# Optimization experiments

Measured on AMD Instinct MI355X. Metric: run time of the kernel, lower is better.

## Reference

```python
import jax, jax.numpy as jnp
import numpy as np

B, S, D = 8, 2048, 1024

def setup_inputs() -> dict:
    key = jax.random.key(0)
    kq, kk, kv = jax.random.split(key, 3)
    qm = jax.random.normal(kq, (B, S, D), dtype=jnp.float32)
    km = jax.random.normal(kk, (B, S, D), dtype=jnp.float32)
    vm = jax.random.normal(kv, (B, S, D), dtype=jnp.float32)
    return {"qm": qm, "km": km, "vm": vm}

def reference(qm, km, vm):
    # qkm = qm @ km^T / sqrt(d_k)   -> [B, S, S]
    scale = 1.0 / jnp.sqrt(jnp.asarray(qm.shape[-1], dtype=qm.dtype))
    qkm = jnp.einsum('bqd,bkd->bqk', qm, km) * scale
    # NOTE: faithful to source: softmax is applied AFTER the second matmul,
    # i.e. softmax((QK^T/sqrt(d)) @ V, axis=-1). masking=False (module default).
    out = jnp.einsum('bqk,bkd->bqd', qkm, vm)  # [B, S, D]
    return jax.nn.softmax(out, axis=-1)
```

## Files before the change

kernel.cpp:

```cpp
#include <hip/hip_runtime.h>
#include <hip/hip_bf16.h>
#include <stdint.h>

#define BATCH 8
#define SEQ   2048
#define DIM   1024

typedef unsigned short u16;
typedef __attribute__((ext_vector_type(8))) short short8;
typedef __attribute__((ext_vector_type(4))) float f32x4;
typedef __attribute__((ext_vector_type(4))) unsigned short us4;

__device__ __forceinline__ u16 f2bf(float x){
  union { float f; uint32_t u; } c; c.f = x;
  uint32_t u = c.u;
  uint32_t r = u + 0x7fffu + ((u >> 16) & 1u);
  return (u16)(r >> 16);
}
__device__ __forceinline__ float bf2f(u16 s){
  union { uint32_t u; float f; } c; c.u = ((uint32_t)s) << 16;
  return c.f;
}

__device__ __forceinline__ void gload16(const void* g, void* l){
  __builtin_amdgcn_global_load_lds(
      (const __attribute__((address_space(1))) void*)g,
      (__attribute__((address_space(3))) void*)l, 16, 0, 0);
}

__global__ __launch_bounds__(256) void k_split(const float* __restrict__ src,
                                               u16* __restrict__ dst, int nchunk){
  for (int i = blockIdx.x*blockDim.x + threadIdx.x; i < nchunk; i += gridDim.x*blockDim.x){
    int r = i >> 8;
    int c = (i & 255) << 2;
    f32x4 v = *(const f32x4*)(src + (size_t)r*DIM + c);
    us4 h, l;
    #pragma unroll
    for (int j = 0; j < 4; j++){
      u16 hh = f2bf(v[j]);
      h[j] = hh;
      l[j] = f2bf(v[j] - bf2f(hh));
    }
    u16* d = dst + (size_t)r*(2*DIM) + c;
    *(us4*)d         = h;
    *(us4*)(d + DIM) = l;
  }
}

__global__ __launch_bounds__(256) void k_convert_kv(const float* __restrict__ K,
                                                    const float* __restrict__ V,
                                                    u16* __restrict__ Kt,
                                                    u16* __restrict__ Vt){
  __shared__ float tile[64][65];
  int z = blockIdx.z;
  const float* Src = (z < 8 ? K : V);
  u16* Dst = (z < 8 ? Kt : Vt);
  int zb = z & 7;
  const float* Vb = Src + (size_t)zb * SEQ * DIM;
  u16* Vtb = Dst + (size_t)zb * DIM * (2*SEQ);
  int s0 = blockIdx.x * 64, d0 = blockIdx.y * 64;
  int t = threadIdx.x;
  int rs = t >> 4;
  int cd = (t & 15) * 4;
  #pragma unroll
  for (int i = 0; i < 4; i++){
    int s = rs + i*16;
    f32x4 v = *(const f32x4*)(Vb + (size_t)(s0 + s)*DIM + d0 + cd);
    tile[s][cd+0] = v[0]; tile[s][cd+1] = v[1];
    tile[s][cd+2] = v[2]; tile[s][cd+3] = v[3];
  }
  __syncthreads();
  int dl = t >> 4;
  int sl = (t & 15) * 4;
  #pragma unroll
  for (int i = 0; i < 4; i++){
    int d = dl + i*16;
    us4 h, l;
    #pragma unroll
    for (int j = 0; j < 4; j++){
      float x = tile[sl+j][d];
      u16 hh = f2bf(x);
      h[j] = hh;
      l[j] = f2bf(x - bf2f(hh));
    }
    size_t off = (size_t)(d0 + d) * (2*SEQ) + s0 + sl;
    *(us4*)(Vtb + off)       = h;
    *(us4*)(Vtb + off + SEQ) = l;
  }
}

template<int N_, int KB, int SPLITOUT, int BX, int RX, int RY>
__global__ __launch_bounds__(256,2) void k_gemm(const u16* __restrict__ A,
                                                const u16* __restrict__ B,
                                                void* __restrict__ Cout,
                                                size_t aStride, size_t bStride, size_t cStride){
  constexpr int LA = 2*KB;
  __shared__ __align__(16) u16 lds[2][4][128*32];

  int orig = blockIdx.x;
  int xcd = orig & 7;
  int idx = orig >> 3;
  constexpr int RN = RX * RY;
  int z  = idx / RN;
  int r  = idx % RN;
  int bx = (xcd % (BX/RX)) * RX + (r % RX);
  int by = (xcd / (BX/RX)) * RY + (r / RX);

  const u16* Ab = A + (size_t)z * aStride;
  const u16* Bb = B + (size_t)z * bStride;

  int t = threadIdx.x, lane = t & 63, w = t >> 6;
  int wm = (w & 1) * 64, wn = (w >> 1) * 64;
  int fr = lane & 15;

  int srow    = lane >> 2;
  int srcSlot = ((lane & 3) ^ ((lane >> 3) & 3)) * 8;

  const u16* aBase = Ab + ((size_t)bx*128) * LA + srcSlot;
  const u16* bBase = Bb + ((size_t)by*128) * LA + srcSlot;

  int rdSlot = (((lane >> 4) ^ ((fr >> 1) & 3))) * 8;

  f32x4 acc[4][4] = {};

  #define STAGE(buf, k0)                                                      \
    { _Pragma("unroll")                                                       \
      for (int o = 0; o < 2; o++){                                            \
        int c = w*2 + o;                                                      \
        size_t rOff = (size_t)(c*16 + srow) * LA + (k0);                      \
        const u16* ga = aBase + rOff;                                         \
        const u16* gb = bBase + rOff;                                         \
        int le = c * 512;                                                     \
        gload16(ga,      &lds[buf][0][le]);                                   \
        gload16(ga + KB, &lds[buf][1][le]);                                   \
        gload16(gb,      &lds[buf][2][le]);                                   \
        gload16(gb + KB, &lds[buf][3][le]);                                   \
      } }

  #define COMPUTE(buf)                                                        \
    { short8 fah[4], fal[4], fbh[4], fbl[4];                                  \
      _Pragma("unroll")                                                       \
      for (int mi = 0; mi < 4; mi++){                                         \
        fah[mi] = *(const short8*)&lds[buf][0][(wm + mi*16 + fr)*32 + rdSlot];\
        fal[mi] = *(const short8*)&lds[buf][1][(wm + mi*16 + fr)*32 + rdSlot];\
        fbh[mi] = *(const short8*)&lds[buf][2][(wn + mi*16 + fr)*32 + rdSlot];\
        fbl[mi] = *(const short8*)&lds[buf][3][(wn + mi*16 + fr)*32 + rdSlot];\
      }                                                                       \
      _Pragma("unroll")                                                       \
      for (int mi = 0; mi < 4; mi++){                                         \
        _Pragma("unroll")                                                     \
        for (int ni = 0; ni < 4; ni++){                                       \
          acc[mi][ni] = __builtin_amdgcn_mfma_f32_16x16x32_bf16(fah[mi], fbh[ni], acc[mi][ni], 0,0,0); \
          acc[mi][ni] = __builtin_amdgcn_mfma_f32_16x16x32_bf16(fah[mi], fbl[ni], acc[mi][ni], 0,0,0); \
          acc[mi][ni] = __builtin_amdgcn_mfma_f32_16x16x32_bf16(fal[mi], fbh[ni], acc[mi][ni], 0,0,0); \
        }                                                                     \
      } }

  STAGE(0, 0)
  int cur = 0;
  for (int k0 = 0; k0 + 32 < KB; k0 += 32, cur ^= 1){
    STAGE(cur^1, k0 + 32)
    asm volatile("s_waitcnt vmcnt(8)" ::: "memory");
    __builtin_amdgcn_sched_barrier(0);
    __builtin_amdgcn_s_barrier();
    __builtin_amdgcn_sched_barrier(0);
    COMPUTE(cur)
    __builtin_amdgcn_sched_barrier(0);
    __builtin_amdgcn_s_barrier();
  }
  asm volatile("s_waitcnt vmcnt(0)" ::: "memory");
  __builtin_amdgcn_sched_barrier(0);
  __builtin_amdgcn_s_barrier();
  __builtin_amdgcn_sched_barrier(0);
  COMPUTE(cur)

  #undef STAGE
  #undef COMPUTE

  int cr = (lane >> 4) * 4, cc = lane & 15;
  if (SPLITOUT){
    u16* Cb = (u16*)Cout + (size_t)z * cStride;
    const float scale = 0.03125f;
    #pragma unroll
    for (int mi = 0; mi < 4; mi++){
      int gr = bx*128 + wm + mi*16 + cr;
      #pragma unroll
      for (int ni = 0; ni < 4; ni++){
        int gc = by*128 + wn + ni*16 + cc;
        #pragma unroll
        for (int rr = 0; rr < 4; rr++){
          float x = acc[mi][ni][rr] * scale;
          u16 h = f2bf(x);
          u16 l = f2bf(x - bf2f(h));
          size_t off = (size_t)(gr + rr) * (2*N_) + gc;
          Cb[off]      = h;
          Cb[off + N_] = l;
        }
      }
    }
  } else {
    float* Cb = (float*)Cout + (size_t)z * cStride;
    #pragma unroll
    for (int mi = 0; mi < 4; mi++){
      int gr = bx*128 + wm + mi*16 + cr;
      #pragma unroll
      for (int ni = 0; ni < 4; ni++){
        int gc = by*128 + wn + ni*16 + cc;
        #pragma unroll
        for (int rr = 0; rr < 4; rr++){
          Cb[(size_t)(gr + rr) * N_ + gc] = acc[mi][ni][rr];
        }
      }
    }
  }
}

__global__ __launch_bounds__(256) void k_softmax(float* __restrict__ O){
  float* p = O + (size_t)blockIdx.x * DIM;
  int t = threadIdx.x;
  int lane = t & 63, wave = t >> 6;
  f32x4 v = *(f32x4*)(p + t*4);
  float m = fmaxf(fmaxf(v[0], v[1]), fmaxf(v[2], v[3]));
  #pragma unroll
  for (int o = 32; o > 0; o >>= 1) m = fmaxf(m, __shfl_xor(m, o));
  __shared__ float rmax[4], rsum[4];
  if (lane == 0) rmax[wave] = m;
  __syncthreads();
  m = fmaxf(fmaxf(rmax[0], rmax[1]), fmaxf(rmax[2], rmax[3]));
  float e0 = expf(v[0]-m), e1 = expf(v[1]-m), e2 = expf(v[2]-m), e3 = expf(v[3]-m);
  float s = e0 + e1 + e2 + e3;
  #pragma unroll
  for (int o = 32; o > 0; o >>= 1) s += __shfl_xor(s, o);
  if (lane == 0) rsum[wave] = s;
  __syncthreads();
  s = rsum[0] + rsum[1] + rsum[2] + rsum[3];
  float inv = 1.0f / s;
  f32x4 rv = { e0*inv, e1*inv, e2*inv, e3*inv };
  *(f32x4*)(p + t*4) = rv;
}

extern "C" void kernel_launch(void* const* d_in, const int* in_sizes, int n_in,
                              void* d_out, int out_size, void* d_ws, size_t ws_size,
                              hipStream_t stream){
  const float* Q = (const float*)d_in[0];
  const float* K = (const float*)d_in[1];
  const float* V = (const float*)d_in[2];
  float* Out = (float*)d_out;
  u16* w = (u16*)d_ws;

  const size_t QsB = (size_t)SEQ * (2*DIM);
  const size_t KtB = (size_t)DIM * (2*SEQ);
  const size_t VtB = KtB;
  const size_t WsB = (size_t)DIM * (2*DIM);

  dim3 blk(256);
  dim3 cgrid(SEQ/64, DIM/64, 16);

  const size_t need1 = 8 * (QsB + KtB + VtB + WsB) * sizeof(u16);
  const size_t need2 = 8 * (KtB + VtB + WsB) * sizeof(u16);

  if (ws_size >= need1){
    u16* Qs = w;
    u16* Kt = Qs + 8*QsB;
    u16* Vt = Kt + 8*KtB;
    u16* Ws = Vt + 8*VtB;
    k_split<<<dim3(2048), blk, 0, stream>>>(Q, Qs, 8*SEQ*(DIM/4));
    k_convert_kv<<<cgrid, blk, 0, stream>>>(K, V, Kt, Vt);
    k_gemm<DIM, SEQ, 1, 8, 2, 4><<<dim3(512), blk, 0, stream>>>(Vt, Kt, Ws, VtB, KtB, WsB);
    k_gemm<DIM, DIM, 0, 16, 4, 4><<<dim3(1024), blk, 0, stream>>>(Qs, Ws, Out, QsB, WsB, (size_t)SEQ*DIM);
  } else if (ws_size >= need2){
    u16* Kt = w;
    u16* Vt = Kt + 8*KtB;
    u16* Ws = Vt + 8*VtB;
    u16* Qs = w;
    k_convert_kv<<<cgrid, blk, 0, stream>>>(K, V, Kt, Vt);
    k_gemm<DIM, SEQ, 1, 8, 2, 4><<<dim3(512), blk, 0, stream>>>(Vt, Kt, Ws, VtB, KtB, WsB);
    k_split<<<dim3(2048), blk, 0, stream>>>(Q, Qs, 8*SEQ*(DIM/4));
    k_gemm<DIM, DIM, 0, 16, 4, 4><<<dim3(1024), blk, 0, stream>>>(Qs, Ws, Out, QsB, WsB, (size_t)SEQ*DIM);
  } else {
    u16* Qs = w;
    u16* Kt = Qs + QsB;
    u16* Vt = Kt + KtB;
    u16* Ws = Vt + VtB;
    dim3 cg1(SEQ/64, DIM/64, 2);
    for (int b = 0; b < BATCH; b++){
      const size_t inOff = (size_t)b * SEQ * DIM;
      k_split<<<dim3(1024), blk, 0, stream>>>(Q + inOff, Qs, SEQ*(DIM/4));
      k_convert_kv<<<dim3(SEQ/64, DIM/64, 1), blk, 0, stream>>>(K + inOff, K + inOff, Kt, Kt);
      k_convert_kv<<<dim3(SEQ/64, DIM/64, 1), blk, 0, stream>>>(V + inOff, V + inOff, Vt, Vt);
      k_gemm<DIM, SEQ, 1, 8, 2, 4><<<dim3(64), blk, 0, stream>>>(Vt, Kt, Ws, VtB, KtB, WsB);
      k_gemm<DIM, DIM, 0, 16, 4, 4><<<dim3(128), blk, 0, stream>>>(Qs, Ws, Out + inOff, QsB, WsB, (size_t)SEQ*DIM);
    }
  }
  k_softmax<<<dim3(BATCH*SEQ), blk, 0, stream>>>(Out);
}
```

Measured before the change: 309.4 us.

## Add 256x256-tile 8-wave GEMM with split-K for KᵀV and reduce kernel

Adds a new GEMM kernel using 512-thread blocks computing 256x256 output tiles with a finer-grained interleaving of LDS fragment loads and MFMA groups, barriers and wave priority raising. The KᵀV product is split into two K-halves written as fp32 partials, then a new reduce kernel sums them, applies the scale, and splits into bf16 hi/lo. The Q·W product also uses the new big-tile kernel. The aim is more operand reuse per tile and better MFMA occupancy, at the cost of an extra partial buffer round-trip, a new launch, and one block per CU with high register pressure.

```diff
diff --git a/kernel.cpp b/kernel.cpp
--- a/kernel.cpp
+++ b/kernel.cpp
@@ -89,11 +89,170 @@
   }
 }
 
+template<int KROW, int SPLITK, int TPZX, int TPZY>
+__global__ __launch_bounds__(512,1) void k_gemm8(const u16* __restrict__ A,
+                                                 const u16* __restrict__ B,
+                                                 float* __restrict__ C,
+                                                 size_t aStride, size_t bStride, size_t cStride){
+  constexpr int LA = 2*KROW;
+  constexpr int NT = 1024/32;
+  __shared__ __align__(16) u16 lds[2][4][256*32];
+
+  int xcd = blockIdx.x & 7;
+  int idx = blockIdx.x >> 3;
+  int nPerX = gridDim.x >> 3;
+  int gid = xcd * nPerX + idx;
+  constexpr int TPZ = TPZX*TPZY;
+  int z  = gid / TPZ;
+  int rm = gid % TPZ;
+  int bx = rm % TPZX;
+  int by = rm / TPZX;
+
+  int zb = SPLITK ? (z & 7) : z;
+  int kh = SPLITK ? (z >> 3) : 0;
+
+  const u16* Ab = A + (size_t)zb * aStride + (size_t)kh * 1024;
+  const u16* Bb = B + (size_t)zb * bStride + (size_t)kh * 1024;
+  float* Cb = C + (size_t)z * cStride;
+
+  int t0 = threadIdx.x, lane = t0 & 63, wv = t0 >> 6;
+  int wm = (wv >> 2) * 128, wn = (wv & 3) * 64;
+  int fr = lane & 15;
+  int rdSlot = ((lane >> 4) ^ ((fr >> 1) & 3)) * 8;
+  int srow = lane >> 2;
+  int srcSlot = ((lane & 3) ^ ((lane >> 3) & 3)) * 8;
+
+  const u16* aB = Ab + ((size_t)bx*256) * LA + srcSlot;
+  const u16* bB = Bb + ((size_t)by*256) * LA + srcSlot;
+  int ldsB0 = wv*512;
+
+  f32x4 acc[8][4] = {};
+  short8 fah[4], fal[4], fbh0[2], fbl0[2], fbh1[2], fbl1[2];
+
+  #define STAGE8(buf, t32)                                                    \
+    { _Pragma("unroll")                                                       \
+      for (int hf = 0; hf < 2; hf++){                                         \
+        size_t ro = (size_t)(wv*16 + hf*128 + srow) * LA + (size_t)(t32)*32;  \
+        const u16* ga = aB + ro;                                              \
+        const u16* gb = bB + ro;                                              \
+        int lo = ldsB0 + hf*4096;                                             \
+        gload16(ga,        &lds[buf][0][lo]);                                 \
+        gload16(ga + KROW, &lds[buf][1][lo]);                                 \
+        gload16(gb,        &lds[buf][2][lo]);                                 \
+        gload16(gb + KROW, &lds[buf][3][lo]);                                 \
+      } }
+
+  #define LOAD_A(buf, h)                                                      \
+    { _Pragma("unroll")                                                       \
+      for (int q = 0; q < 4; q++){                                            \
+        int ra = (wm + ((h)*4+q)*16 + fr)*32 + rdSlot;                        \
+        fah[q] = *(const short8*)&lds[buf][0][ra];                            \
+        fal[q] = *(const short8*)&lds[buf][1][ra];                            \
+      } }
+  #define LOAD_B0(buf)                                                        \
+    { _Pragma("unroll")                                                       \
+      for (int q = 0; q < 2; q++){                                            \
+        int rb = (wn + q*16 + fr)*32 + rdSlot;                                \
+        fbh0[q] = *(const short8*)&lds[buf][2][rb];                           \
+        fbl0[q] = *(const short8*)&lds[buf][3][rb];                           \
+      } }
+  #define LOAD_B1(buf)                                                        \
+    { _Pragma("unroll")                                                       \
+      for (int q = 0; q < 2; q++){                                            \
+        int rb = (wn + (2+q)*16 + fr)*32 + rdSlot;                            \
+        fbh1[q] = *(const short8*)&lds[buf][2][rb];                           \
+        fbl1[q] = *(const short8*)&lds[buf][3][rb];                           \
+      } }
+
+  #define MFMA_Q(h, bh, bl, nb)                                               \
+    { _Pragma("unroll")                                                       \
+      for (int q = 0; q < 4; q++){                                            \
+        _Pragma("unroll")                                                     \
+        for (int j = 0; j < 2; j++){                                          \
+          f32x4 a0 = acc[(h)*4+q][(nb)+j];                                    \
+          a0 = __builtin_amdgcn_mfma_f32_16x16x32_bf16(fah[q], bh[j], a0, 0,0,0); \
+          a0 = __builtin_amdgcn_mfma_f32_16x16x32_bf16(fah[q], bl[j], a0, 0,0,0); \
+          a0 = __builtin_amdgcn_mfma_f32_16x16x32_bf16(fal[q], bh[j], a0, 0,0,0); \
+          acc[(h)*4+q][(nb)+j] = a0;                                          \
+        } } }
+
+  #define BARR()  __builtin_amdgcn_s_barrier()
+  #define LGKM0() { asm volatile("s_waitcnt lgkmcnt(0)" ::: "memory"); __builtin_amdgcn_sched_barrier(0); }
+  #define VMC0()  { asm volatile("s_waitcnt vmcnt(0)" ::: "memory"); __builtin_amdgcn_sched_barrier(0); }
+
+  STAGE8(0, 0)
+  VMC0()
+  BARR();
+
+  for (int t = 0; t < NT; t++){
+    int buf = t & 1;
+    if (t+1 < NT) STAGE8(buf^1, t+1)
+    LOAD_A(buf, 0) LOAD_B0(buf)
+    BARR(); LGKM0()
+    __builtin_amdgcn_s_setprio(1); MFMA_Q(0, fbh0, fbl0, 0) __builtin_amdgcn_s_setprio(0);
+    BARR();
+    LOAD_B1(buf)
+    BARR(); LGKM0()
+    __builtin_amdgcn_s_setprio(1); MFMA_Q(0, fbh1, fbl1, 2) __builtin_amdgcn_s_setprio(0);
+    BARR();
+    LOAD_A(buf, 1)
+    BARR(); LGKM0()
+    __builtin_amdgcn_s_setprio(1); MFMA_Q(1, fbh1, fbl1, 2) __builtin_amdgcn_s_setprio(0);
+    BARR();
+    __builtin_amdgcn_s_setprio(1); MFMA_Q(1, fbh0, fbl0, 0) __builtin_amdgcn_s_setprio(0);
+    if (t+1 < NT) VMC0()
+    BARR();
+  }
+
+  #undef STAGE8
+  #undef LOAD_A
+  #undef LOAD_B0
+  #undef LOAD_B1
+  #undef MFMA_Q
+  #undef BARR
+  #undef LGKM0
+  #undef VMC0
+
+  int cr = (lane >> 4) * 4;
+  #pragma unroll
+  for (int mi = 0; mi < 8; mi++){
+    int gr = bx*256 + wm + mi*16 + cr;
+    #pragma unroll
+    for (int ni = 0; ni < 4; ni++){
+      int gc = by*256 + wn + ni*16 + fr;
+      #pragma unroll
+      for (int e = 0; e < 4; e++)
+        Cb[(size_t)(gr + e) * 1024 + gc] = acc[mi][ni][e];
+    }
+  }
+}
+
+__global__ __launch_bounds__(256) void k_reduce_split(const float* __restrict__ P,
+                                                      u16* __restrict__ Ws){
+  int i = blockIdx.x*256 + threadIdx.x;
+  int rg = i >> 8;
+  int c  = (i & 255) * 4;
+  f32x4 a = *(const f32x4*)(P + (size_t)rg*1024 + c);
+  f32x4 b = *(const f32x4*)(P + ((size_t)rg + 8192)*1024 + c);
+  us4 h, l;
+  #pragma unroll
+  for (int j = 0; j < 4; j++){
+    float x = (a[j] + b[j]) * 0.03125f;
+    u16 hh = f2bf(x);
+    h[j] = hh;
+    l[j] = f2bf(x - bf2f(hh));
+  }
+  int zb = rg >> 10, d = rg & 1023;
+  u16* Wb = Ws + (size_t)zb * ((size_t)DIM * 2*DIM);
+  *(us4*)(Wb + (size_t)d*2048 + c)        = h;
+  *(us4*)(Wb + (size_t)d*2048 + 1024 + c) = l;
+}
+
 template<int N_, int KB, int SPLITOUT, int BX, int RX, int RY>
-__global__ __launch_bounds__(256,2) void k_gemm(const u16* __restrict__ A,
-                                                const u16* __restrict__ B,
-                                                void* __restrict__ Cout,
-                                                size_t aStride, size_t bStride, size_t cStride){
+__global__ __launch_bounds__(256,2) void k_gemm2ph(const u16* __restrict__ A,
+                                                   const u16* __restrict__ B,
+                                                   void* __restrict__ Cout,
+                                                   size_t aStride, size_t bStride, size_t cStride){
   constexpr int LA = 2*KB;
   __shared__ __align__(16) u16 lds[2][4][128*32];
 
@@ -112,13 +271,11 @@
   int t = threadIdx.x, lane = t & 63, w = t >> 6;
   int wm = (w & 1) * 64, wn = (w >> 1) * 64;
   int fr = lane & 15;
-
   int srow    = lane >> 2;
   int srcSlot = ((lane & 3) ^ ((lane >> 3) & 3)) * 8;
 
   const u16* aBase = Ab + ((size_t)bx*128) * LA + srcSlot;
   const u16* bBase = Bb + ((size_t)by*128) * LA + srcSlot;
-
   int rdSlot = (((lane >> 4) ^ ((fr >> 1) & 3))) * 8;
 
   f32x4 acc[4][4] = {};
@@ -256,40 +413,45 @@
   dim3 blk(256);
   dim3 cgrid(SEQ/64, DIM/64, 16);
 
-  const size_t need1 = 8 * (QsB + KtB + VtB + WsB) * sizeof(u16);
-  const size_t need2 = 8 * (KtB + VtB + WsB) * sizeof(u16);
-
-  if (ws_size >= need1){
-    u16* Qs = w;
-    u16* Kt = Qs + 8*QsB;
+  const size_t base2 = 8 * (KtB + VtB + WsB) * sizeof(u16);
+  const size_t needA = base2 + (size_t)16*1024*1024*sizeof(float);
+  const size_t needB = base2;
+
+  if (ws_size >= needA){
+    u16* Kt = w;
     u16* Vt = Kt + 8*KtB;
     u16* Ws = Vt + 8*VtB;
+    float* Part = (float*)(Ws + 8*WsB);
+    u16* Qs = w;
+    k_convert_kv<<<cgrid, blk, 0, stream>>>(K, V, Kt, Vt);
+    k_gemm8<SEQ, 1, 4, 4><<<dim3(256), dim3(512), 0, stream>>>(
+        Vt, Kt, Part, VtB, KtB, (size_t)1024*1024);
+    k_reduce_split<<<dim3(8192), blk, 0, stream>>>(Part, Ws);
     k_split<<<dim3(2048), blk, 0, stream>>>(Q, Qs, 8*SEQ*(DIM/4));
-    k_convert_kv<<<cgrid, blk, 0, stream>>>(K, V, Kt, Vt);
-    k_gemm<DIM, SEQ, 1, 8, 2, 4><<<dim3(512), blk, 0, stream>>>(Vt, Kt, Ws, VtB, KtB, WsB);
-    k_gemm<DIM, DIM, 0, 16, 4, 4><<<dim3(1024), blk, 0, stream>>>(Qs, Ws, Out, QsB, WsB, (size_t)SEQ*DIM);
-  } else if (ws_size >= need2){
+    k_gemm8<DIM, 0, 8, 4><<<dim3(256), dim3(512), 0, stream>>>(
+        Qs, Ws, Out, QsB, WsB, (size_t)SEQ*DIM);
+  } else if (ws_size >= needB){
     u16* Kt = w;
     u16* Vt = Kt + 8*KtB;
     u16* Ws = Vt + 8*VtB;
     u16* Qs = w;
     k_convert_kv<<<cgrid, blk, 0, stream>>>(K, V, Kt, Vt);
-    k_gemm<DIM, SEQ, 1, 8, 2, 4><<<dim3(512), blk, 0, stream>>>(Vt, Kt, Ws, VtB, KtB, WsB);
+    k_gemm2ph<DIM, SEQ, 1, 8, 2, 4><<<dim3(512), blk, 0, stream>>>(Vt, Kt, Ws, VtB, KtB, WsB);
     k_split<<<dim3(2048), blk, 0, stream>>>(Q, Qs, 8*SEQ*(DIM/4));
-    k_gemm<DIM, DIM, 0, 16, 4, 4><<<dim3(1024), blk, 0, stream>>>(Qs, Ws, Out, QsB, WsB, (size_t)SEQ*DIM);
+    k_gemm8<DIM, 0, 8, 4><<<dim3(256), dim3(512), 0, stream>>>(
+        Qs, Ws, Out, QsB, WsB, (size_t)SEQ*DIM);
   } else {
     u16* Qs = w;
     u16* Kt = Qs + QsB;
     u16* Vt = Kt + KtB;
     u16* Ws = Vt + VtB;
-    dim3 cg1(SEQ/64, DIM/64, 2);
     for (int b = 0; b < BATCH; b++){
       const size_t inOff = (size_t)b * SEQ * DIM;
       k_split<<<dim3(1024), blk, 0, stream>>>(Q + inOff, Qs, SEQ*(DIM/4));
       k_convert_kv<<<dim3(SEQ/64, DIM/64, 1), blk, 0, stream>>>(K + inOff, K + inOff, Kt, Kt);
       k_convert_kv<<<dim3(SEQ/64, DIM/64, 1), blk, 0, stream>>>(V + inOff, V + inOff, Vt, Vt);
-      k_gemm<DIM, SEQ, 1, 8, 2, 4><<<dim3(64), blk, 0, stream>>>(Vt, Kt, Ws, VtB, KtB, WsB);
-      k_gemm<DIM, DIM, 0, 16, 4, 4><<<dim3(128), blk, 0, stream>>>(Qs, Ws, Out + inOff, QsB, WsB, (size_t)SEQ*DIM);
+      k_gemm2ph<DIM, SEQ, 1, 8, 2, 4><<<dim3(64), blk, 0, stream>>>(Vt, Kt, Ws, VtB, KtB, WsB);
+      k_gemm2ph<DIM, DIM, 0, 16, 4, 4><<<dim3(128), blk, 0, stream>>>(Qs, Ws, Out + inOff, QsB, WsB, (size_t)SEQ*DIM);
     }
   }
   k_softmax<<<dim3(BATCH*SEQ), blk, 0, stream>>>(Out);
```

Measured after the change: 285.4 us. 7.8% less time.

## Enlarge GEMM tiles to 128/256x256 with wave-level sub-blocking and drop Q-split-first path

Applied to the files above, without the earlier changes.

Replaces the 128x128-tile split-bf16 GEMM with a templated kernel that uses 128x256 or 256x256 block tiles, one block per CU, and 64x128 or 128x128 per-wave tiles. A and B fragments are loaded in sub-blocks to limit register pressure. The larger tiles raise arithmetic intensity and cut LDS and global traffic per MFMA. The cost is fewer blocks (256), which gives coarser load balance across CUs, plus higher register use and lower occupancy. The workspace path that split Q before computing K^T V is removed, so the smaller-workspace ordering is now always used.

```diff
diff --git a/kernel.cpp b/kernel.cpp
--- a/kernel.cpp
+++ b/kernel.cpp
@@ -26,6 +26,13 @@
   __builtin_amdgcn_global_load_lds(
       (const __attribute__((address_space(1))) void*)g,
       (__attribute__((address_space(3))) void*)l, 16, 0, 0);
+}
+
+__device__ __forceinline__ f32x4 mfma3(short8 ah, short8 al, short8 bh, short8 bl, f32x4 c){
+  c = __builtin_amdgcn_mfma_f32_16x16x32_bf16(ah, bh, c, 0,0,0);
+  c = __builtin_amdgcn_mfma_f32_16x16x32_bf16(ah, bl, c, 0,0,0);
+  c = __builtin_amdgcn_mfma_f32_16x16x32_bf16(al, bh, c, 0,0,0);
+  return c;
 }
 
 __global__ __launch_bounds__(256) void k_split(const float* __restrict__ src,
@@ -89,127 +96,158 @@
   }
 }
 
-template<int N_, int KB, int SPLITOUT, int BX, int RX, int RY>
-__global__ __launch_bounds__(256,2) void k_gemm(const u16* __restrict__ A,
-                                                const u16* __restrict__ B,
-                                                void* __restrict__ Cout,
-                                                size_t aStride, size_t bStride, size_t cStride){
-  constexpr int LA = 2*KB;
-  __shared__ __align__(16) u16 lds[2][4][128*32];
-
-  int orig = blockIdx.x;
-  int xcd = orig & 7;
-  int idx = orig >> 3;
-  constexpr int RN = RX * RY;
-  int z  = idx / RN;
-  int r  = idx % RN;
-  int bx = (xcd % (BX/RX)) * RX + (r % RX);
-  int by = (xcd / (BX/RX)) * RY + (r / RX);
+template<int BM, int KROW, int SPLITOUT, int NOUT, int TPZX, int TPZY>
+__global__ __launch_bounds__(256,1) void k_gemm4(const u16* __restrict__ A,
+                                                 const u16* __restrict__ B,
+                                                 void* __restrict__ Cout,
+                                                 size_t aStride, size_t bStride, size_t cStride){
+  constexpr int LA  = 2*KROW;
+  constexpr int NT  = KROW/32;
+  constexpr int AF  = BM/32;
+  constexpr int NAG = AF/4;
+  constexpr int ACH = BM/64;
+  constexpr int NLD = 2*ACH + 8;
+  constexpr int OAL = BM*32;
+  constexpr int OBH = 2*BM*32;
+  constexpr int OBL = 2*BM*32 + 8192;
+  constexpr int LDSPB = 2*BM*32 + 16384;
+
+  __shared__ __align__(16) u16 lds[2][LDSPB];
+
+  int xcd = blockIdx.x & 7;
+  int idx = blockIdx.x >> 3;
+  int nPerX = gridDim.x >> 3;
+  int gid = xcd * nPerX + idx;
+  constexpr int TPZ = TPZX*TPZY;
+  int z  = gid / TPZ;
+  int rm = gid % TPZ;
+  int bx = rm % TPZX;
+  int by = rm / TPZX;
 
   const u16* Ab = A + (size_t)z * aStride;
   const u16* Bb = B + (size_t)z * bStride;
 
-  int t = threadIdx.x, lane = t & 63, w = t >> 6;
-  int wm = (w & 1) * 64, wn = (w >> 1) * 64;
+  int t0 = threadIdx.x, lane = t0 & 63, wv = t0 >> 6;
+  int wm = (wv >> 1) * (BM/2);
+  int wn = (wv & 1) * 128;
   int fr = lane & 15;
-
-  int srow    = lane >> 2;
+  int rdSlot = ((lane >> 4) ^ ((fr >> 1) & 3)) * 8;
+  int srow4 = lane >> 2;
   int srcSlot = ((lane & 3) ^ ((lane >> 3) & 3)) * 8;
 
-  const u16* aBase = Ab + ((size_t)bx*128) * LA + srcSlot;
-  const u16* bBase = Bb + ((size_t)by*128) * LA + srcSlot;
-
-  int rdSlot = (((lane >> 4) ^ ((fr >> 1) & 3))) * 8;
-
-  f32x4 acc[4][4] = {};
-
-  #define STAGE(buf, k0)                                                      \
-    { _Pragma("unroll")                                                       \
-      for (int o = 0; o < 2; o++){                                            \
-        int c = w*2 + o;                                                      \
-        size_t rOff = (size_t)(c*16 + srow) * LA + (k0);                      \
-        const u16* ga = aBase + rOff;                                         \
-        const u16* gb = bBase + rOff;                                         \
-        int le = c * 512;                                                     \
-        gload16(ga,      &lds[buf][0][le]);                                   \
-        gload16(ga + KB, &lds[buf][1][le]);                                   \
-        gload16(gb,      &lds[buf][2][le]);                                   \
-        gload16(gb + KB, &lds[buf][3][le]);                                   \
-      } }
-
-  #define COMPUTE(buf)                                                        \
-    { short8 fah[4], fal[4], fbh[4], fbl[4];                                  \
+  const u16* aB = Ab + ((size_t)bx*BM)  * LA + srcSlot;
+  const u16* bB = Bb + ((size_t)by*256) * LA + srcSlot;
+
+  f32x4 acc[AF][8] = {};
+  short8 aH[4], aL[4], bH[4], bL[4];
+
+  #define STAGE(buf, t32)                                                     \
+    { size_t kof = (size_t)(t32)*32;                                          \
       _Pragma("unroll")                                                       \
-      for (int mi = 0; mi < 4; mi++){                                         \
-        fah[mi] = *(const short8*)&lds[buf][0][(wm + mi*16 + fr)*32 + rdSlot];\
-        fal[mi] = *(const short8*)&lds[buf][1][(wm + mi*16 + fr)*32 + rdSlot];\
-        fbh[mi] = *(const short8*)&lds[buf][2][(wn + mi*16 + fr)*32 + rdSlot];\
-        fbl[mi] = *(const short8*)&lds[buf][3][(wn + mi*16 + fr)*32 + rdSlot];\
+      for (int c = 0; c < ACH; c++){                                          \
+        size_t ro = (size_t)(c*64 + wv*16 + srow4)*LA + kof;                  \
+        gload16(aB + ro,        &lds[buf][      c*2048 + wv*512]);            \
+        gload16(aB + KROW + ro, &lds[buf][OAL + c*2048 + wv*512]);            \
       }                                                                       \
       _Pragma("unroll")                                                       \
-      for (int mi = 0; mi < 4; mi++){                                         \
+      for (int c = 0; c < 4; c++){                                            \
+        size_t ro = (size_t)(c*64 + wv*16 + srow4)*LA + kof;                  \
+        gload16(bB + ro,        &lds[buf][OBH + c*2048 + wv*512]);            \
+        gload16(bB + KROW + ro, &lds[buf][OBL + c*2048 + wv*512]);            \
+      } }
+
+  #define LOAD_A(buf, ag)                                                     \
+    { _Pragma("unroll")                                                       \
+      for (int q = 0; q < 4; q++){                                            \
+        int ra = (wm + (ag)*64 + q*16 + fr)*32 + rdSlot;                      \
+        aH[q] = *(const short8*)&lds[buf][ra];                                \
+        aL[q] = *(const short8*)&lds[buf][OAL + ra];                          \
+      } }
+  #define LOAD_B(buf, bh)                                                     \
+    { _Pragma("unroll")                                                       \
+      for (int q = 0; q < 4; q++){                                            \
+        int rb = (wn + (bh)*64 + q*16 + fr)*32 + rdSlot;                      \
+        bH[q] = *(const short8*)&lds[buf][OBH + rb];                          \
+        bL[q] = *(const short8*)&lds[buf][OBL + rb];                          \
+      } }
+  #define MFMA_BLK(ag, bh)                                                    \
+    { _Pragma("unroll")                                                       \
+      for (int q = 0; q < 4; q++){                                            \
         _Pragma("unroll")                                                     \
-        for (int ni = 0; ni < 4; ni++){                                       \
-          acc[mi][ni] = __builtin_amdgcn_mfma_f32_16x16x32_bf16(fah[mi], fbh[ni], acc[mi][ni], 0,0,0); \
-          acc[mi][ni] = __builtin_amdgcn_mfma_f32_16x16x32_bf16(fah[mi], fbl[ni], acc[mi][ni], 0,0,0); \
-          acc[mi][ni] = __builtin_amdgcn_mfma_f32_16x16x32_bf16(fal[mi], fbh[ni], acc[mi][ni], 0,0,0); \
-        }                                                                     \
-      } }
+        for (int j = 0; j < 4; j++){                                          \
+          acc[(ag)*4+q][(bh)*4+j] =                                           \
+            mfma3(aH[q], aL[q], bH[j], bL[j], acc[(ag)*4+q][(bh)*4+j]);       \
+        } } }
+
+  #define SB0() __builtin_amdgcn_sched_barrier(0)
 
   STAGE(0, 0)
-  int cur = 0;
-  for (int k0 = 0; k0 + 32 < KB; k0 += 32, cur ^= 1){
-    STAGE(cur^1, k0 + 32)
-    asm volatile("s_waitcnt vmcnt(8)" ::: "memory");
-    __builtin_amdgcn_sched_barrier(0);
+  asm volatile("s_waitcnt vmcnt(0)" ::: "memory");
+  __builtin_amdgcn_s_barrier();
+  SB0();
+
+  for (int t = 0; t < NT; t++){
+    int buf = t & 1;
+    if (t+1 < NT){
+      STAGE(buf^1, t+1)
+      asm volatile("s_waitcnt vmcnt(%0)" :: "i"(NLD) : "memory");
+    } else {
+      asm volatile("s_waitcnt vmcnt(0)" ::: "memory");
+    }
     __builtin_amdgcn_s_barrier();
-    __builtin_amdgcn_sched_barrier(0);
-    COMPUTE(cur)
-    __builtin_amdgcn_sched_barrier(0);
+    SB0();
+    #pragma unroll
+    for (int bh = 0; bh < 2; bh++){
+      LOAD_B(buf, bh)
+      #pragma unroll
+      for (int ag = 0; ag < NAG; ag++){
+        LOAD_A(buf, ag)
+        MFMA_BLK(ag, bh)
+      }
+    }
+    SB0();
     __builtin_amdgcn_s_barrier();
-  }
-  asm volatile("s_waitcnt vmcnt(0)" ::: "memory");
-  __builtin_amdgcn_sched_barrier(0);
-  __builtin_amdgcn_s_barrier();
-  __builtin_amdgcn_sched_barrier(0);
-  COMPUTE(cur)
+    SB0();
+  }
 
   #undef STAGE
-  #undef COMPUTE
-
-  int cr = (lane >> 4) * 4, cc = lane & 15;
+  #undef LOAD_A
+  #undef LOAD_B
+  #undef MFMA_BLK
+  #undef SB0
+
+  int cr = (lane >> 4) * 4;
   if (SPLITOUT){
     u16* Cb = (u16*)Cout + (size_t)z * cStride;
     const float scale = 0.03125f;
     #pragma unroll
-    for (int mi = 0; mi < 4; mi++){
-      int gr = bx*128 + wm + mi*16 + cr;
+    for (int mi = 0; mi < AF; mi++){
+      int gr = bx*BM + wm + mi*16 + cr;
       #pragma unroll
-      for (int ni = 0; ni < 4; ni++){
-        int gc = by*128 + wn + ni*16 + cc;
+      for (int ni = 0; ni < 8; ni++){
+        int gc = by*256 + wn + ni*16 + fr;
         #pragma unroll
-        for (int rr = 0; rr < 4; rr++){
-          float x = acc[mi][ni][rr] * scale;
+        for (int e = 0; e < 4; e++){
+          float x = acc[mi][ni][e] * scale;
           u16 h = f2bf(x);
           u16 l = f2bf(x - bf2f(h));
-          size_t off = (size_t)(gr + rr) * (2*N_) + gc;
-          Cb[off]      = h;
-          Cb[off + N_] = l;
+          size_t off = (size_t)(gr + e) * (2*NOUT) + gc;
+          Cb[off]        = h;
+          Cb[off + NOUT] = l;
         }
       }
     }
   } else {
     float* Cb = (float*)Cout + (size_t)z * cStride;
     #pragma unroll
-    for (int mi = 0; mi < 4; mi++){
-      int gr = bx*128 + wm + mi*16 + cr;
+    for (int mi = 0; mi < AF; mi++){
+      int gr = bx*BM + wm + mi*16 + cr;
       #pragma unroll
-      for (int ni = 0; ni < 4; ni++){
-        int gc = by*128 + wn + ni*16 + cc;
+      for (int ni = 0; ni < 8; ni++){
+        int gc = by*256 + wn + ni*16 + fr;
         #pragma unroll
-        for (int rr = 0; rr < 4; rr++){
-          Cb[(size_t)(gr + rr) * N_ + gc] = acc[mi][ni][rr];
-        }
+        for (int e = 0; e < 4; e++)
+          Cb[(size_t)(gr + e) * NOUT + gc] = acc[mi][ni][e];
       }
     }
   }
@@ -256,40 +294,33 @@
   dim3 blk(256);
   dim3 cgrid(SEQ/64, DIM/64, 16);
 
-  const size_t need1 = 8 * (QsB + KtB + VtB + WsB) * sizeof(u16);
-  const size_t need2 = 8 * (KtB + VtB + WsB) * sizeof(u16);
-
-  if (ws_size >= need1){
-    u16* Qs = w;
-    u16* Kt = Qs + 8*QsB;
-    u16* Vt = Kt + 8*KtB;
-    u16* Ws = Vt + 8*VtB;
-    k_split<<<dim3(2048), blk, 0, stream>>>(Q, Qs, 8*SEQ*(DIM/4));
-    k_convert_kv<<<cgrid, blk, 0, stream>>>(K, V, Kt, Vt);
-    k_gemm<DIM, SEQ, 1, 8, 2, 4><<<dim3(512), blk, 0, stream>>>(Vt, Kt, Ws, VtB, KtB, WsB);
-    k_gemm<DIM, DIM, 0, 16, 4, 4><<<dim3(1024), blk, 0, stream>>>(Qs, Ws, Out, QsB, WsB, (size_t)SEQ*DIM);
-  } else if (ws_size >= need2){
+  const size_t need = 8 * (KtB + VtB + WsB) * sizeof(u16);
+
+  if (ws_size >= need){
     u16* Kt = w;
     u16* Vt = Kt + 8*KtB;
     u16* Ws = Vt + 8*VtB;
     u16* Qs = w;
     k_convert_kv<<<cgrid, blk, 0, stream>>>(K, V, Kt, Vt);
-    k_gemm<DIM, SEQ, 1, 8, 2, 4><<<dim3(512), blk, 0, stream>>>(Vt, Kt, Ws, VtB, KtB, WsB);
+    k_gemm4<128, SEQ, 1, DIM, 8, 4><<<dim3(256), blk, 0, stream>>>(
+        Vt, Kt, Ws, VtB, KtB, WsB);
     k_split<<<dim3(2048), blk, 0, stream>>>(Q, Qs, 8*SEQ*(DIM/4));
-    k_gemm<DIM, DIM, 0, 16, 4, 4><<<dim3(1024), blk, 0, stream>>>(Qs, Ws, Out, QsB, WsB, (size_t)SEQ*DIM);
+    k_gemm4<256, DIM, 0, DIM, 8, 4><<<dim3(256), blk, 0, stream>>>(
+        Qs, Ws, Out, QsB, WsB, (size_t)SEQ*DIM);
   } else {
     u16* Qs = w;
     u16* Kt = Qs + QsB;
     u16* Vt = Kt + KtB;
     u16* Ws = Vt + VtB;
-    dim3 cg1(SEQ/64, DIM/64, 2);
     for (int b = 0; b < BATCH; b++){
       const size_t inOff = (size_t)b * SEQ * DIM;
       k_split<<<dim3(1024), blk, 0, stream>>>(Q + inOff, Qs, SEQ*(DIM/4));
       k_convert_kv<<<dim3(SEQ/64, DIM/64, 1), blk, 0, stream>>>(K + inOff, K + inOff, Kt, Kt);
       k_convert_kv<<<dim3(SEQ/64, DIM/64, 1), blk, 0, stream>>>(V + inOff, V + inOff, Vt, Vt);
-      k_gemm<DIM, SEQ, 1, 8, 2, 4><<<dim3(64), blk, 0, stream>>>(Vt, Kt, Ws, VtB, KtB, WsB);
-      k_gemm<DIM, DIM, 0, 16, 4, 4><<<dim3(128), blk, 0, stream>>>(Qs, Ws, Out + inOff, QsB, WsB, (size_t)SEQ*DIM);
+      k_gemm4<128, SEQ, 1, DIM, 8, 4><<<dim3(32), blk, 0, stream>>>(
+          Vt, Kt, Ws, VtB, KtB, WsB);
+      k_gemm4<256, DIM, 0, DIM, 8, 4><<<dim3(32), blk, 0, stream>>>(
+          Qs, Ws, Out + inOff, QsB, WsB, (size_t)SEQ*DIM);
     }
   }
   k_softmax<<<dim3(BATCH*SEQ), blk, 0, stream>>>(Out);
```

After: 291.0 us. -6.0%, faster.

## Split-K the V^T·K GEMM, single-buffer LDS at higher occupancy

Applied to the files above, without the earlier changes.

The first GEMM (V^T K, K dimension 2048) is split into two K halves that write fp32 partials. A new reduction kernel sums the halves, scales them and writes the bf16 hi/lo split weight matrix. This doubles block count and parallelism for the small 1024x1024 output. The GEMM kernel drops the double-buffered LDS prefetch pipeline for a single buffer with __syncthreads and launch_bounds occupancy 4, relying on more resident blocks to hide latency. Block-index swizzling is simplified to a linear per-XCD mapping. This costs extra partial-sum traffic and one more launch, and loses explicit load/compute overlap.

```diff
diff --git a/kernel.cpp b/kernel.cpp
--- a/kernel.cpp
+++ b/kernel.cpp
@@ -89,25 +89,30 @@
   }
 }
 
-template<int N_, int KB, int SPLITOUT, int BX, int RX, int RY>
-__global__ __launch_bounds__(256,2) void k_gemm(const u16* __restrict__ A,
-                                                const u16* __restrict__ B,
-                                                void* __restrict__ Cout,
-                                                size_t aStride, size_t bStride, size_t cStride){
-  constexpr int LA = 2*KB;
-  __shared__ __align__(16) u16 lds[2][4][128*32];
-
-  int orig = blockIdx.x;
-  int xcd = orig & 7;
-  int idx = orig >> 3;
-  constexpr int RN = RX * RY;
-  int z  = idx / RN;
-  int r  = idx % RN;
-  int bx = (xcd % (BX/RX)) * RX + (r % RX);
-  int by = (xcd / (BX/RX)) * RY + (r / RX);
-
-  const u16* Ab = A + (size_t)z * aStride;
-  const u16* Bb = B + (size_t)z * bStride;
+template<int KROW, int SPLITK, int SPLITOUT, int NOUT, int TX, int TY>
+__global__ __launch_bounds__(256,4) void k_gemmS(const u16* __restrict__ A,
+                                                 const u16* __restrict__ B,
+                                                 void* __restrict__ Cout,
+                                                 size_t aStride, size_t bStride, size_t cStride){
+  constexpr int LA = 2*KROW;
+  constexpr int ITER = (SPLITK ? 1024 : KROW) / 32;
+  __shared__ __align__(16) u16 lds[4][128*32];
+
+  int xcd = blockIdx.x & 7;
+  int idx = blockIdx.x >> 3;
+  int nPerX = gridDim.x >> 3;
+  int gid = xcd * nPerX + idx;
+  constexpr int TPZ = TX*TY;
+  int z  = gid / TPZ;
+  int rm = gid % TPZ;
+  int bx = rm % TX;
+  int by = rm / TX;
+
+  int zb = SPLITK ? (z & 7) : z;
+  int kh = SPLITK ? (z >> 3) : 0;
+
+  const u16* Ab = A + (size_t)zb * aStride + (size_t)kh * 1024;
+  const u16* Bb = B + (size_t)zb * bStride + (size_t)kh * 1024;
 
   int t = threadIdx.x, lane = t & 63, w = t >> 6;
   int wm = (w & 1) * 64, wn = (w >> 1) * 64;
@@ -123,59 +128,41 @@
 
   f32x4 acc[4][4] = {};
 
-  #define STAGE(buf, k0)                                                      \
-    { _Pragma("unroll")                                                       \
-      for (int o = 0; o < 2; o++){                                            \
-        int c = w*2 + o;                                                      \
-        size_t rOff = (size_t)(c*16 + srow) * LA + (k0);                      \
-        const u16* ga = aBase + rOff;                                         \
-        const u16* gb = bBase + rOff;                                         \
-        int le = c * 512;                                                     \
-        gload16(ga,      &lds[buf][0][le]);                                   \
-        gload16(ga + KB, &lds[buf][1][le]);                                   \
-        gload16(gb,      &lds[buf][2][le]);                                   \
-        gload16(gb + KB, &lds[buf][3][le]);                                   \
-      } }
-
-  #define COMPUTE(buf)                                                        \
-    { short8 fah[4], fal[4], fbh[4], fbl[4];                                  \
-      _Pragma("unroll")                                                       \
-      for (int mi = 0; mi < 4; mi++){                                         \
-        fah[mi] = *(const short8*)&lds[buf][0][(wm + mi*16 + fr)*32 + rdSlot];\
-        fal[mi] = *(const short8*)&lds[buf][1][(wm + mi*16 + fr)*32 + rdSlot];\
-        fbh[mi] = *(const short8*)&lds[buf][2][(wn + mi*16 + fr)*32 + rdSlot];\
-        fbl[mi] = *(const short8*)&lds[buf][3][(wn + mi*16 + fr)*32 + rdSlot];\
-      }                                                                       \
-      _Pragma("unroll")                                                       \
-      for (int mi = 0; mi < 4; mi++){                                         \
-        _Pragma("unroll")                                                     \
-        for (int ni = 0; ni < 4; ni++){                                       \
-          acc[mi][ni] = __builtin_amdgcn_mfma_f32_16x16x32_bf16(fah[mi], fbh[ni], acc[mi][ni], 0,0,0); \
-          acc[mi][ni] = __builtin_amdgcn_mfma_f32_16x16x32_bf16(fah[mi], fbl[ni], acc[mi][ni], 0,0,0); \
-          acc[mi][ni] = __builtin_amdgcn_mfma_f32_16x16x32_bf16(fal[mi], fbh[ni], acc[mi][ni], 0,0,0); \
-        }                                                                     \
-      } }
-
-  STAGE(0, 0)
-  int cur = 0;
-  for (int k0 = 0; k0 + 32 < KB; k0 += 32, cur ^= 1){
-    STAGE(cur^1, k0 + 32)
-    asm volatile("s_waitcnt vmcnt(8)" ::: "memory");
-    __builtin_amdgcn_sched_barrier(0);
-    __builtin_amdgcn_s_barrier();
-    __builtin_amdgcn_sched_barrier(0);
-    COMPUTE(cur)
-    __builtin_amdgcn_sched_barrier(0);
-    __builtin_amdgcn_s_barrier();
-  }
-  asm volatile("s_waitcnt vmcnt(0)" ::: "memory");
-  __builtin_amdgcn_sched_barrier(0);
-  __builtin_amdgcn_s_barrier();
-  __builtin_amdgcn_sched_barrier(0);
-  COMPUTE(cur)
-
-  #undef STAGE
-  #undef COMPUTE
+  for (int ti = 0; ti < ITER; ti++){
+    size_t kof = (size_t)ti * 32;
+    #pragma unroll
+    for (int o = 0; o < 2; o++){
+      int c = w*2 + o;
+      size_t ro = (size_t)(c*16 + srow) * LA + kof;
+      const u16* ga = aBase + ro;
+      const u16* gb = bBase + ro;
+      int le = c * 512;
+      gload16(ga,        &lds[0][le]);
+      gload16(ga + KROW, &lds[1][le]);
+      gload16(gb,        &lds[2][le]);
+      gload16(gb + KROW, &lds[3][le]);
+    }
+    __syncthreads();
+
+    short8 fah[4], fal[4], fbh[4], fbl[4];
+    #pragma unroll
+    for (int mi = 0; mi < 4; mi++){
+      fah[mi] = *(const short8*)&lds[0][(wm + mi*16 + fr)*32 + rdSlot];
+      fal[mi] = *(const short8*)&lds[1][(wm + mi*16 + fr)*32 + rdSlot];
+      fbh[mi] = *(const short8*)&lds[2][(wn + mi*16 + fr)*32 + rdSlot];
+      fbl[mi] = *(const short8*)&lds[3][(wn + mi*16 + fr)*32 + rdSlot];
+    }
+    #pragma unroll
+    for (int mi = 0; mi < 4; mi++){
+      #pragma unroll
+      for (int ni = 0; ni < 4; ni++){
+        acc[mi][ni] = __builtin_amdgcn_mfma_f32_16x16x32_bf16(fah[mi], fbh[ni], acc[mi][ni], 0,0,0);
+        acc[mi][ni] = __builtin_amdgcn_mfma_f32_16x16x32_bf16(fah[mi], fbl[ni], acc[mi][ni], 0,0,0);
+        acc[mi][ni] = __builtin_amdgcn_mfma_f32_16x16x32_bf16(fal[mi], fbh[ni], acc[mi][ni], 0,0,0);
+      }
+    }
+    __syncthreads();
+  }
 
   int cr = (lane >> 4) * 4, cc = lane & 15;
   if (SPLITOUT){
@@ -192,9 +179,9 @@
           float x = acc[mi][ni][rr] * scale;
           u16 h = f2bf(x);
           u16 l = f2bf(x - bf2f(h));
-          size_t off = (size_t)(gr + rr) * (2*N_) + gc;
-          Cb[off]      = h;
-          Cb[off + N_] = l;
+          size_t off = (size_t)(gr + rr) * (2*NOUT) + gc;
+          Cb[off]        = h;
+          Cb[off + NOUT] = l;
         }
       }
     }
@@ -208,11 +195,32 @@
         int gc = by*128 + wn + ni*16 + cc;
         #pragma unroll
         for (int rr = 0; rr < 4; rr++){
-          Cb[(size_t)(gr + rr) * N_ + gc] = acc[mi][ni][rr];
+          Cb[(size_t)(gr + rr) * NOUT + gc] = acc[mi][ni][rr];
         }
       }
     }
   }
+}
+
+__global__ __launch_bounds__(256) void k_reduce_split(const float* __restrict__ P,
+                                                      u16* __restrict__ Ws){
+  int i = blockIdx.x*256 + threadIdx.x;
+  int rg = i >> 8;
+  int c  = (i & 255) * 4;
+  f32x4 a = *(const f32x4*)(P + (size_t)rg*1024 + c);
+  f32x4 b = *(const f32x4*)(P + ((size_t)rg + 8192)*1024 + c);
+  us4 h, l;
+  #pragma unroll
+  for (int j = 0; j < 4; j++){
+    float x = (a[j] + b[j]) * 0.03125f;
+    u16 hh = f2bf(x);
+    h[j] = hh;
+    l[j] = f2bf(x - bf2f(hh));
+  }
+  int zb = rg >> 10, d = rg & 1023;
+  u16* Wb = Ws + (size_t)zb * ((size_t)DIM * 2*DIM);
+  *(us4*)(Wb + (size_t)d*2048 + c)        = h;
+  *(us4*)(Wb + (size_t)d*2048 + 1024 + c) = l;
 }
 
 __global__ __launch_bounds__(256) void k_softmax(float* __restrict__ O){
@@ -256,40 +264,48 @@
   dim3 blk(256);
   dim3 cgrid(SEQ/64, DIM/64, 16);
 
-  const size_t need1 = 8 * (QsB + KtB + VtB + WsB) * sizeof(u16);
-  const size_t need2 = 8 * (KtB + VtB + WsB) * sizeof(u16);
-
-  if (ws_size >= need1){
-    u16* Qs = w;
-    u16* Kt = Qs + 8*QsB;
+  const size_t base2 = 8 * (KtB + VtB + WsB) * sizeof(u16);
+  const size_t needA = base2 + (size_t)16*1024*1024*sizeof(float);
+  const size_t needB = base2;
+
+  if (ws_size >= needA){
+    u16* Kt = w;
     u16* Vt = Kt + 8*KtB;
     u16* Ws = Vt + 8*VtB;
+    float* Part = (float*)(Ws + 8*WsB);
+    u16* Qs = w;
+    k_convert_kv<<<cgrid, blk, 0, stream>>>(K, V, Kt, Vt);
+    k_gemmS<SEQ, 1, 0, DIM, 8, 8><<<dim3(1024), blk, 0, stream>>>(
+        Vt, Kt, Part, VtB, KtB, (size_t)1024*1024);
+    k_reduce_split<<<dim3(8192), blk, 0, stream>>>(Part, Ws);
     k_split<<<dim3(2048), blk, 0, stream>>>(Q, Qs, 8*SEQ*(DIM/4));
-    k_convert_kv<<<cgrid, blk, 0, stream>>>(K, V, Kt, Vt);
-    k_gemm<DIM, SEQ, 1, 8, 2, 4><<<dim3(512), blk, 0, stream>>>(Vt, Kt, Ws, VtB, KtB, WsB);
-    k_gemm<DIM, DIM, 0, 16, 4, 4><<<dim3(1024), blk, 0, stream>>>(Qs, Ws, Out, QsB, WsB, (size_t)SEQ*DIM);
-  } else if (ws_size >= need2){
+    k_gemmS<DIM, 0, 0, DIM, 16, 8><<<dim3(1024), blk, 0, stream>>>(
+        Qs, Ws, Out, QsB, WsB, (size_t)SEQ*DIM);
+  } else if (ws_size >= needB){
     u16* Kt = w;
     u16* Vt = Kt + 8*KtB;
     u16* Ws = Vt + 8*VtB;
     u16* Qs = w;
     k_convert_kv<<<cgrid, blk, 0, stream>>>(K, V, Kt, Vt);
-    k_gemm<DIM, SEQ, 1, 8, 2, 4><<<dim3(512), blk, 0, stream>>>(Vt, Kt, Ws, VtB, KtB, WsB);
+    k_gemmS<SEQ, 0, 1, DIM, 8, 8><<<dim3(512), blk, 0, stream>>>(
+        Vt, Kt, Ws, VtB, KtB, WsB);
     k_split<<<dim3(2048), blk, 0, stream>>>(Q, Qs, 8*SEQ*(DIM/4));
-    k_gemm<DIM, DIM, 0, 16, 4, 4><<<dim3(1024), blk, 0, stream>>>(Qs, Ws, Out, QsB, WsB, (size_t)SEQ*DIM);
+    k_gemmS<DIM, 0, 0, DIM, 16, 8><<<dim3(1024), blk, 0, stream>>>(
+        Qs, Ws, Out, QsB, WsB, (size_t)SEQ*DIM);
   } else {
     u16* Qs = w;
     u16* Kt = Qs + QsB;
     u16* Vt = Kt + KtB;
     u16* Ws = Vt + VtB;
-    dim3 cg1(SEQ/64, DIM/64, 2);
     for (int b = 0; b < BATCH; b++){
       const size_t inOff = (size_t)b * SEQ * DIM;
       k_split<<<dim3(1024), blk, 0, stream>>>(Q + inOff, Qs, SEQ*(DIM/4));
       k_convert_kv<<<dim3(SEQ/64, DIM/64, 1), blk, 0, stream>>>(K + inOff, K + inOff, Kt, Kt);
       k_convert_kv<<<dim3(SEQ/64, DIM/64, 1), blk, 0, stream>>>(V + inOff, V + inOff, Vt, Vt);
-      k_gemm<DIM, SEQ, 1, 8, 2, 4><<<dim3(64), blk, 0, stream>>>(Vt, Kt, Ws, VtB, KtB, WsB);
-      k_gemm<DIM, DIM, 0, 16, 4, 4><<<dim3(128), blk, 0, stream>>>(Qs, Ws, Out + inOff, QsB, WsB, (size_t)SEQ*DIM);
+      k_gemmS<SEQ, 0, 1, DIM, 8, 8><<<dim3(64), blk, 0, stream>>>(
+          Vt, Kt, Ws, VtB, KtB, WsB);
+      k_gemmS<DIM, 0, 0, DIM, 16, 8><<<dim3(128), blk, 0, stream>>>(
+          Qs, Ws, Out + inOff, QsB, WsB, (size_t)SEQ*DIM);
     }
   }
   k_softmax<<<dim3(BATCH*SEQ), blk, 0, stream>>>(Out);
```

Result: no change. 313.7 us (+1.4%).
